# Kernel optimization log

Hardware: AMD Instinct MI355X
Metric: run time of the kernel (lower is better)

Reference implementation:

```python
import jax, jax.numpy as jnp
import numpy as np

B, S, DM = 4, 2048, 1024
H, HD = 16, 64  # num_heads, head_dimension


def setup_inputs() -> dict:
    key = jax.random.key(0)
    ks = jax.random.split(key, 11)
    s = 0.02
    return {
        "queries": jax.random.normal(ks[0], (B, S, DM), dtype=jnp.float32),
        "keys": jax.random.normal(ks[1], (B, S, DM), dtype=jnp.float32),
        "values": jax.random.normal(ks[2], (B, S, DM), dtype=jnp.float32),
        # projection params, stored [in, out] (transpose of torch Linear weight)
        "Wq": jax.random.normal(ks[3], (DM, H * HD), dtype=jnp.float32) * s,
        "bq": jnp.zeros((H * HD,), dtype=jnp.float32),
        "Wk": jax.random.normal(ks[4], (DM, H * HD), dtype=jnp.float32) * s,
        "bk": jnp.zeros((H * HD,), dtype=jnp.float32),
        "Wv": jax.random.normal(ks[5], (DM, H * HD), dtype=jnp.float32) * s,
        "bv": jnp.zeros((H * HD,), dtype=jnp.float32),
        "Wo": jax.random.normal(ks[6], (H * HD, DM), dtype=jnp.float32) * s,
        "bo": jnp.zeros((DM,), dtype=jnp.float32),
    }


def reference(queries, keys, values, Wq, bq, Wk, bk, Wv, bv, Wo, bo):
    b, s, _ = queries.shape
    # project and split heads: [b, s, H*HD] -> [b, H, s, HD]
    def split(x):
        return x.reshape(b, s, H, HD).transpose(0, 2, 1, 3)
    q = split(queries @ Wq + bq)
    k = split(keys @ Wk + bk)
    v = split(values @ Wv + bv)
    # raw scores [b, H, sq, sk]
    attn = jnp.einsum("bhqd,bhkd->bhqk", q, k)
    # FAITHFUL to source: mask is a no-op (masked_fill result discarded);
    # softmax over axis=2 (the QUERY axis), then scaled by 1/sqrt(HD) after.
    attn = jax.nn.softmax(attn, axis=2) / jnp.sqrt(jnp.float32(HD))
    out = jnp.einsum("bhqk,bhkd->bhqd", attn, v)  # [b, H, s, HD]
    out = out.transpose(0, 2, 1, 3).reshape(b, s, H * HD)
    return out @ Wo + bo
```

## Files before the change

### kernel.cpp

```cpp
#include <hip/hip_runtime.h>
#include <cstddef>


typedef unsigned short u16t;
typedef __attribute__((ext_vector_type(8))) short short8;
typedef __attribute__((ext_vector_type(4))) float floatx4;
typedef __attribute__((ext_vector_type(4))) unsigned int uintx4;

#define MFMA16(a, b, c) __builtin_amdgcn_mfma_f32_16x16x32_bf16((a), (b), (c), 0, 0, 0)
#define GLDS16(g, l)                                                        \
  __builtin_amdgcn_global_load_lds(                                         \
      (const __attribute__((address_space(1))) unsigned int*)(g),           \
      (__attribute__((address_space(3))) unsigned int*)(l), 16, 0, 0)

#if __has_builtin(__builtin_amdgcn_exp2f)
#define EXP2(x) __builtin_amdgcn_exp2f(x)
#else
#define EXP2(x) __expf(0.69314718f * (x))
#endif

static __device__ __forceinline__ u16t f2bf(float f) {
  union { float f; unsigned u; } v; v.f = f;
  unsigned r = v.u + 0x7FFFu + ((v.u >> 16) & 1u);
  return (u16t)(r >> 16);
}
static __device__ __forceinline__ unsigned pack2(float hi, float lo) {
  union { float f; unsigned u; } a, b; a.f = hi; b.f = lo;
  return __builtin_amdgcn_perm(a.u + 0x8000u, b.u + 0x8000u, 0x07060302u);
}
static __device__ __forceinline__ unsigned cvtpk(float lo, float hi) {
  unsigned r;
  asm("v_cvt_pk_bf16_f32 %0, %1, %2" : "=v"(r) : "v"(lo), "v"(hi));
  return r;
}

static __device__ __forceinline__ int swz(int row, int col) {
  return (((col >> 3) ^ (row & 7)) << 3) | (col & 7);
}

#define SEQ    2048
#define NHEAD  16
#define HDIM   64
#define DMODEL 1024

__global__ __launch_bounds__(256)
void wt_kernel(const float* __restrict__ W0, const float* __restrict__ W1,
               const float* __restrict__ W2, const float* __restrict__ W3,
               u16t* __restrict__ T0, u16t* __restrict__ T1,
               u16t* __restrict__ T2, u16t* __restrict__ T3) {
  int id = blockIdx.x * 256 + threadIdx.x;
  int wsel = id >> 17;
  int r = id & 131071;
  int n = r & 1023;
  int k0 = (r >> 10) << 3;
  const float* W = wsel == 0 ? W0 : wsel == 1 ? W1 : wsel == 2 ? W2 : W3;
  u16t* T = wsel == 0 ? T0 : wsel == 1 ? T1 : wsel == 2 ? T2 : T3;
  const float* src = W + (size_t)k0 * 1024 + n;
  float f[8];
#pragma unroll
  for (int i = 0; i < 8; ++i) f[i] = src[(size_t)i * 1024];
  uint4 p;
  p.x = pack2(f[1], f[0]); p.y = pack2(f[3], f[2]);
  p.z = pack2(f[5], f[4]); p.w = pack2(f[7], f[6]);
  *(uint4*)&T[(size_t)n * 1024 + (k0 & ~63) + swz(n, k0 & 63)] = p;
}

__global__ __launch_bounds__(256)
void cvt_kernel(const float* __restrict__ X0, const float* __restrict__ X1,
                u16t* __restrict__ T0, u16t* __restrict__ T1) {
  int id = blockIdx.x * 256 + threadIdx.x;
  int wsel = id >> 20;
  int r = id & 1048575;
  int m = r >> 7;
  int k0 = (r & 127) << 3;
  const float* X = wsel == 0 ? X0 : X1;
  u16t* T = wsel == 0 ? T0 : T1;
  const float4* src = (const float4*)(X + (size_t)m * 1024 + k0);
  float4 a = src[0], b = src[1];
  uint4 p;
  p.x = pack2(a.y, a.x); p.y = pack2(a.w, a.z);
  p.z = pack2(b.y, b.x); p.w = pack2(b.w, b.z);
  *(uint4*)&T[(size_t)m * 1024 + (k0 & ~63) + swz(m, k0 & 63)] = p;
}

template <int MODE>
__global__ __launch_bounds__(256)
void gemm_bt(const void* __restrict__ Ap0, const void* __restrict__ Ap1,
             const u16t* __restrict__ BT0, const u16t* __restrict__ BT1,
             const float* __restrict__ bias0, const float* __restrict__ bias1,
             void* __restrict__ Cp0, void* __restrict__ Cp1,
             float sc0, float sc1, const float* __restrict__ sscv) {
  constexpr int K = 1024;
  __shared__ __align__(16) u16t lA[128 * 64];
  __shared__ __align__(16) u16t lB[128 * 64];
  const int z = blockIdx.z;
  const void* Ap = z ? Ap1 : Ap0;
  const u16t* BT = z ? BT1 : BT0;
  const float* bias = z ? bias1 : bias0;
  void* Cp = z ? Cp1 : Cp0;
  const float qsc = z ? sc1 : sc0;
  const int tid = threadIdx.x;
  const int lane = tid & 63, w = tid >> 6;
  const int wm = w >> 1, wn = w & 1;
  const int lrow = lane & 15, lq = lane >> 4;
  const int raw = blockIdx.y * 8 + blockIdx.x;
  const int xcd = raw & 7, slot = raw >> 3;
  const int m0 = (xcd * 8 + (slot >> 3)) * 128;
  const int n0 = (slot & 7) * 128;

  floatx4 acc[4][4];
#pragma unroll
  for (int i = 0; i < 4; ++i)
#pragma unroll
    for (int j = 0; j < 4; ++j) acc[i][j] = {0.f, 0.f, 0.f, 0.f};

  for (int kb = 0; kb < K; kb += 64) {
    if constexpr (MODE == 2) {
      const float* Ag = (const float*)Ap;
#pragma unroll
      for (int i = 0; i < 8; ++i) {
        int e = (i * 256 + tid) * 4;
        int r = e >> 6, c = e & 63;
        const float* src = Ag + (size_t)(m0 + r) * K + kb + c;
        uint2 p;
        p.x = pack2(src[1], src[0]);
        p.y = pack2(src[3], src[2]);
        *(uint2*)&lA[r * 64 + swz(r, c)] = p;
      }
    } else {
      const u16t* Ag = (const u16t*)Ap;
#pragma unroll
      for (int i = 0; i < 4; ++i) {
        int chunk = w * 4 + i;
        int off = chunk * 1024 + lane * 16;
        int r = off >> 7, ib = off & 127;
        GLDS16(Ag + (size_t)(m0 + r) * K + kb + (ib >> 1), &lA[chunk * 512]);
      }
    }
#pragma unroll
    for (int i = 0; i < 4; ++i) {
      int chunk = w * 4 + i;
      int off = chunk * 1024 + lane * 16;
      int r = off >> 7, ib = off & 127;
      GLDS16(BT + (size_t)(n0 + r) * K + kb + (ib >> 1), &lB[chunk * 512]);
    }
    __syncthreads();
#pragma unroll
    for (int kk = 0; kk < 2; ++kk) {
      short8 af[4], bfr[4];
#pragma unroll
      for (int t = 0; t < 4; ++t) {
        int ar = wm * 64 + t * 16 + lrow;
        af[t] = *(const short8*)&lA[ar * 64 + swz(ar, kk * 32 + lq * 8)];
      }
#pragma unroll
      for (int t = 0; t < 4; ++t) {
        int br = wn * 64 + t * 16 + lrow;
        bfr[t] = *(const short8*)&lB[br * 64 + swz(br, kk * 32 + lq * 8)];
      }
#pragma unroll
      for (int i = 0; i < 4; ++i)
#pragma unroll
        for (int j = 0; j < 4; ++j)
          acc[i][j] = MFMA16(af[i], bfr[j], acc[i][j]);
    }
    __syncthreads();
  }

  float bvv[4];
#pragma unroll
  for (int j = 0; j < 4; ++j) bvv[j] = bias[n0 + wn * 64 + j * 16 + lrow];
  const int h = (n0 + wn * 64) >> 6;
#pragma unroll
  for (int i = 0; i < 4; ++i) {
#pragma unroll
    for (int r = 0; r < 4; ++r) {
      int rg = m0 + wm * 64 + i * 16 + lq * 4 + r;
      int b = rg >> 11, s = rg & 2047;
      float rs;
      if constexpr (MODE == 2) rs = sscv[(size_t)(b * NHEAD + h) * SEQ + s];
      else                     rs = qsc;
#pragma unroll
      for (int j = 0; j < 4; ++j) {
        int cg = n0 + wn * 64 + j * 16 + lrow;
        float v = acc[i][j][r] + bvv[j];
        if constexpr (MODE == 1) {
          ((float*)Cp)[(size_t)rg * 1024 + cg] = v;
        } else {
          v *= rs;
          int d = cg & 63;
          size_t bh = (size_t)(b * NHEAD + h);
          if constexpr (MODE == 0) {
            ((u16t*)Cp)[(bh * SEQ + s) * HDIM + swz(s, d)] = f2bf(v);
          } else {
            int sp = (s & ~31) | (((s >> 2) & 3) << 3) | (s & 3) |
                     (((s >> 4) & 1) << 2);
            ((u16t*)Cp)[(bh * HDIM + d) * SEQ + (s & ~127) + swz(d, sp & 127)] =
                f2bf(v);
          }
        }
      }
    }
  }
}

__global__ __launch_bounds__(256)
void stats_kernel(const u16t* __restrict__ Qb, const u16t* __restrict__ Kb,
                  float* __restrict__ ss) {
  __shared__ __align__(16) u16t lK[128 * 64];
  __shared__ __align__(16) u16t lQ[128 * 64];
  const int tid = threadIdx.x, lane = tid & 63, w = tid >> 6;
  const int lrow = lane & 15, lq = lane >> 4;
  const int bh = blockIdx.x;
  const int c0 = blockIdx.y * 128;
  const u16t* Kbase = Kb + (size_t)bh * (SEQ * HDIM);
  const u16t* Qbase = Qb + (size_t)bh * (SEQ * HDIM);

#pragma unroll
  for (int i = 0; i < 4; ++i) {
    int chunk = w * 4 + i;
    GLDS16(Kbase + (size_t)c0 * HDIM + chunk * 512 + lane * 8, &lK[chunk * 512]);
  }

  short8 bfK[4];
  float lcur[2] = {0.f, 0.f};

  for (int q0 = 0; q0 < SEQ; q0 += 128) {
#pragma unroll
    for (int i = 0; i < 4; ++i) {
      int chunk = w * 4 + i;
      GLDS16(Qbase + (size_t)q0 * HDIM + chunk * 512 + lane * 8, &lQ[chunk * 512]);
    }
    __syncthreads();
    if (q0 == 0) {
#pragma unroll
      for (int nt = 0; nt < 2; ++nt) {
        int kr = w * 32 + nt * 16 + lrow;
        bfK[nt * 2]     = *(const short8*)&lK[kr * 64 + swz(kr, lq * 8)];
        bfK[nt * 2 + 1] = *(const short8*)&lK[kr * 64 + swz(kr, lq * 8 + 32)];
      }
    }
#pragma unroll
    for (int mt = 0; mt < 8; ++mt) {
      int qr = mt * 16 + lrow;
      short8 af0 = *(const short8*)&lQ[qr * 64 + swz(qr, lq * 8)];
      short8 af1 = *(const short8*)&lQ[qr * 64 + swz(qr, lq * 8 + 32)];
#pragma unroll
      for (int nt = 0; nt < 2; ++nt) {
        floatx4 a = {0.f, 0.f, 0.f, 0.f};
        a = MFMA16(af0, bfK[nt * 2], a);
        a = MFMA16(af1, bfK[nt * 2 + 1], a);
        lcur[nt] += EXP2(a[0]) + EXP2(a[1]) + EXP2(a[2]) + EXP2(a[3]);
      }
    }
    __syncthreads();
  }
#pragma unroll
  for (int t = 0; t < 2; ++t) {
    float ll = lcur[t];
    ll += __shfl_xor(ll, 16);
    ll += __shfl_xor(ll, 32);
    lcur[t] = ll;
  }
  if (lane < 16) {
#pragma unroll
    for (int t = 0; t < 2; ++t) {
      int col = c0 + w * 32 + t * 16 + lane;
      ss[(size_t)bh * SEQ + col] = 1.f / (8.f * lcur[t]);
    }
  }
}

__global__ __launch_bounds__(256, 2)
void attn_kernel(const u16t* __restrict__ Qb, const u16t* __restrict__ Kb,
                 const u16t* __restrict__ Vt, u16t* __restrict__ Hout) {
  __shared__ __align__(16) u16t sK[2][8192];
  __shared__ __align__(16) u16t sV[2][8192];
  const int tid = threadIdx.x, lane = tid & 63, w = tid >> 6;
  const int lrow = lane & 15, lq = lane >> 4;
  const int bh = blockIdx.x, q0 = blockIdx.y * 256;
  const size_t hb = (size_t)bh * (SEQ * HDIM);

  auto stage = [&](int t) {
    u16t* dK = sK[t & 1];
    u16t* dV = sV[t & 1];
    const int k0 = t << 7;
#pragma unroll
    for (int i = 0; i < 4; ++i) {
      int chunk = w * 4 + i;
      GLDS16(Kb + hb + (size_t)k0 * HDIM + chunk * 512 + lane * 8, &dK[chunk * 512]);
    }
#pragma unroll
    for (int i = 0; i < 4; ++i) {
      int chunk = w * 4 + i;
      int off = chunk * 1024 + lane * 16;
      int d = off >> 8, ib = off & 255;
      GLDS16(Vt + hb + ((size_t)d << 11) + k0 + (ib >> 1), &dV[chunk * 512]);
    }
  };
  auto loadK = [&](short8 dst[2][2], const u16t* K_, int kw) {
#pragma unroll
    for (int t = 0; t < 2; ++t) {
      int kr = (kw * 2 + t) * 16 + lrow;
      dst[t][0] = *(const short8*)&K_[kr * 64 + swz(kr, lq * 8)];
      dst[t][1] = *(const short8*)&K_[kr * 64 + swz(kr, lq * 8 + 32)];
    }
  };
  auto loadV = [&](short8 dst[4], const u16t* V_, int kw) {
#pragma unroll
    for (int dt = 0; dt < 4; ++dt) {
      int vr = dt * 16 + lrow;
      dst[dt] = *(const short8*)&V_[vr * 128 + swz(vr, kw * 32 + lq * 8)];
    }
  };

  u16t* qs = (u16t*)sK;
#pragma unroll
  for (int i = 0; i < 8; ++i) {
    int chunk = w * 8 + i;
    GLDS16(Qb + hb + (size_t)q0 * HDIM + chunk * 512 + lane * 8, &qs[chunk * 512]);
  }
  __syncthreads();
  short8 bq[4][2];
#pragma unroll
  for (int j = 0; j < 4; ++j) {
    int qr = w * 64 + j * 16 + lrow;
    bq[j][0] = *(const short8*)&qs[qr * 64 + swz(qr, lq * 8)];
    bq[j][1] = *(const short8*)&qs[qr * 64 + swz(qr, lq * 8 + 32)];
  }
  __syncthreads();

  floatx4 ao[4][4];
#pragma unroll
  for (int j = 0; j < 4; ++j)
#pragma unroll
    for (int t = 0; t < 4; ++t) ao[j][t] = {0.f, 0.f, 0.f, 0.f};

  stage(0);
  stage(1);

#pragma unroll 2
  for (int kt = 0; kt < 16; ++kt) {
    if (kt < 15) asm volatile("s_waitcnt vmcnt(8)" ::: "memory");
    else         asm volatile("s_waitcnt vmcnt(0)" ::: "memory");
    __builtin_amdgcn_s_barrier();
    const u16t* K_ = sK[kt & 1];
    const u16t* V_ = sV[kt & 1];

    short8 ak[2][2][2];
    short8 bv[2][4];
    loadK(ak[0], K_, 0);
    loadV(bv[0], V_, 0);

#pragma unroll
    for (int kw = 0; kw < 4; ++kw) {
      const int cb = kw & 1, nb = cb ^ 1;
      if (kw < 3) {
        loadK(ak[nb], K_, kw + 1);
        loadV(bv[nb], V_, kw + 1);
      }
      short8 pa[4];
#pragma unroll
      for (int j = 0; j < 4; ++j) {
        floatx4 s0 = {0.f, 0.f, 0.f, 0.f}, s1 = {0.f, 0.f, 0.f, 0.f};
        __builtin_amdgcn_s_setprio(1);
        s0 = MFMA16(ak[cb][0][0], bq[j][0], s0);
        s0 = MFMA16(ak[cb][0][1], bq[j][1], s0);
        s1 = MFMA16(ak[cb][1][0], bq[j][0], s1);
        s1 = MFMA16(ak[cb][1][1], bq[j][1], s1);
        __builtin_amdgcn_s_setprio(0);
        uintx4 pw;
        pw[0] = cvtpk(EXP2(s0[0]), EXP2(s0[1]));
        pw[1] = cvtpk(EXP2(s0[2]), EXP2(s0[3]));
        pw[2] = cvtpk(EXP2(s1[0]), EXP2(s1[1]));
        pw[3] = cvtpk(EXP2(s1[2]), EXP2(s1[3]));
        pa[j] = __builtin_bit_cast(short8, pw);
      }
      __builtin_amdgcn_s_setprio(1);
#pragma unroll
      for (int dt = 0; dt < 4; ++dt)
#pragma unroll
        for (int j = 0; j < 4; ++j)
          ao[j][dt] = MFMA16(pa[j], bv[cb][dt], ao[j][dt]);
      __builtin_amdgcn_s_setprio(0);
    }

    asm volatile("s_waitcnt lgkmcnt(0)" ::: "memory");
    __builtin_amdgcn_s_barrier();
    if (kt < 14) stage(kt + 2);
  }

  const int b = bh >> 4, h = bh & 15;
#pragma unroll
  for (int j = 0; j < 4; ++j)
#pragma unroll
    for (int dt = 0; dt < 4; ++dt) {
      int d = dt * 16 + lrow;
#pragma unroll
      for (int r = 0; r < 4; ++r) {
        int q = q0 + w * 64 + j * 16 + lq * 4 + r;
        Hout[((size_t)b * SEQ + q) * DMODEL + h * HDIM + swz(q, d)] = f2bf(ao[j][dt][r]);
      }
    }
}

extern "C" void kernel_launch(void* const* d_in, const int* in_sizes, int n_in,
                              void* d_out, int out_size, void* d_ws, size_t ws_size,
                              hipStream_t stream) {
  (void)in_sizes; (void)n_in; (void)out_size; (void)ws_size;
  const float* queries = (const float*)d_in[0];
  const float* keys    = (const float*)d_in[1];
  const float* values  = (const float*)d_in[2];
  const float* Wq = (const float*)d_in[3];
  const float* bq = (const float*)d_in[4];
  const float* Wk = (const float*)d_in[5];
  const float* bk = (const float*)d_in[6];
  const float* Wv = (const float*)d_in[7];
  const float* bv = (const float*)d_in[8];
  const float* Wo = (const float*)d_in[9];
  const float* bo = (const float*)d_in[10];

  char* ws = (char*)d_ws;
  const size_t MB = 1024 * 1024;
  u16t* Qb   = (u16t*)(ws + 0 * MB);
  u16t* Kb   = (u16t*)(ws + 16 * MB);
  u16t* qcv  = (u16t*)(ws + 32 * MB);
  u16t* Hout = qcv;
  u16t* kcv  = (u16t*)(ws + 48 * MB);
  u16t* Vt   = kcv;
  u16t* wqt  = (u16t*)(ws + 64 * MB);
  u16t* wkt  = (u16t*)(ws + 66 * MB);
  u16t* wvt  = (u16t*)(ws + 68 * MB);
  u16t* wot  = (u16t*)(ws + 70 * MB);
  float* ssc = (float*)(ws + 72 * MB);

  wt_kernel<<<2048, 256, 0, stream>>>(Wq, Wk, Wv, Wo, wqt, wkt, wvt, wot);

  cvt_kernel<<<8192, 256, 0, stream>>>(queries, keys, qcv, kcv);

  gemm_bt<0><<<dim3(8, 64, 2), 256, 0, stream>>>(
      qcv, kcv, wqt, wkt, bq, bk, Qb, Kb, 1.44269504f, 1.0f, nullptr);

  stats_kernel<<<dim3(64, 16), 256, 0, stream>>>(Qb, Kb, ssc);

  gemm_bt<2><<<dim3(8, 64, 1), 256, 0, stream>>>(
      values, values, wvt, wvt, bv, bv, Vt, Vt, 1.0f, 1.0f, ssc);

  attn_kernel<<<dim3(64, 8), 256, 0, stream>>>(Qb, Kb, Vt, Hout);

  gemm_bt<1><<<dim3(8, 64, 1), 256, 0, stream>>>(
      Hout, Hout, wot, wot, bo, bo, d_out, d_out, 1.0f, 1.0f, nullptr);
}
```

Before: 379.8 us.

## Software-pipeline QK and exp across kw steps; pre-convert values to bf16

Inside the attention loop, the QK^T MFMAs for the next key sub-tile are now issued before the PV MFMAs of the current one. The exp/convert epilogue runs afterwards, so transcendental work can overlap matrix-core work. Separately, the V projection GEMM no longer converts fp32 values to bf16 inline with scalar loads. A dedicated cvt_kernel pass now pre-converts them, which lets that GEMM use the same direct global-to-LDS loads as the other modes. This adds an extra kernel launch and a round trip through memory, and the extra live score registers may raise register pressure.

Measured after the change: 377.4 us. About the same (-0.6%).

```diff
diff --git a/kernel.cpp b/kernel.cpp
--- a/kernel.cpp
+++ b/kernel.cpp
@@ -66,15 +66,10 @@
 }
 
 __global__ __launch_bounds__(256)
-void cvt_kernel(const float* __restrict__ X0, const float* __restrict__ X1,
-                u16t* __restrict__ T0, u16t* __restrict__ T1) {
+void cvt_kernel(const float* __restrict__ X, u16t* __restrict__ T) {
   int id = blockIdx.x * 256 + threadIdx.x;
-  int wsel = id >> 20;
-  int r = id & 1048575;
-  int m = r >> 7;
-  int k0 = (r & 127) << 3;
-  const float* X = wsel == 0 ? X0 : X1;
-  u16t* T = wsel == 0 ? T0 : T1;
+  int m = id >> 7;
+  int k0 = (id & 127) << 3;
   const float4* src = (const float4*)(X + (size_t)m * 1024 + k0);
   float4 a = src[0], b = src[1];
   uint4 p;
@@ -85,7 +80,7 @@
 
 template <int MODE>
 __global__ __launch_bounds__(256)
-void gemm_bt(const void* __restrict__ Ap0, const void* __restrict__ Ap1,
+void gemm_bt(const u16t* __restrict__ Ap0, const u16t* __restrict__ Ap1,
              const u16t* __restrict__ BT0, const u16t* __restrict__ BT1,
              const float* __restrict__ bias0, const float* __restrict__ bias1,
              void* __restrict__ Cp0, void* __restrict__ Cp1,
@@ -94,7 +89,7 @@
   __shared__ __align__(16) u16t lA[128 * 64];
   __shared__ __align__(16) u16t lB[128 * 64];
   const int z = blockIdx.z;
-  const void* Ap = z ? Ap1 : Ap0;
+  const u16t* Ag = z ? Ap1 : Ap0;
   const u16t* BT = z ? BT1 : BT0;
   const float* bias = z ? bias1 : bias0;
   void* Cp = z ? Cp1 : Cp0;
@@ -115,33 +110,12 @@
     for (int j = 0; j < 4; ++j) acc[i][j] = {0.f, 0.f, 0.f, 0.f};
 
   for (int kb = 0; kb < K; kb += 64) {
-    if constexpr (MODE == 2) {
-      const float* Ag = (const float*)Ap;
-#pragma unroll
-      for (int i = 0; i < 8; ++i) {
-        int e = (i * 256 + tid) * 4;
-        int r = e >> 6, c = e & 63;
-        const float* src = Ag + (size_t)(m0 + r) * K + kb + c;
-        uint2 p;
-        p.x = pack2(src[1], src[0]);
-        p.y = pack2(src[3], src[2]);
-        *(uint2*)&lA[r * 64 + swz(r, c)] = p;
-      }
-    } else {
-      const u16t* Ag = (const u16t*)Ap;
-#pragma unroll
-      for (int i = 0; i < 4; ++i) {
-        int chunk = w * 4 + i;
-        int off = chunk * 1024 + lane * 16;
-        int r = off >> 7, ib = off & 127;
-        GLDS16(Ag + (size_t)(m0 + r) * K + kb + (ib >> 1), &lA[chunk * 512]);
-      }
-    }
 #pragma unroll
     for (int i = 0; i < 4; ++i) {
       int chunk = w * 4 + i;
       int off = chunk * 1024 + lane * 16;
       int r = off >> 7, ib = off & 127;
+      GLDS16(Ag + (size_t)(m0 + r) * K + kb + (ib >> 1), &lA[chunk * 512]);
       GLDS16(BT + (size_t)(n0 + r) * K + kb + (ib >> 1), &lB[chunk * 512]);
     }
     __syncthreads();
@@ -330,6 +304,31 @@
   }
   __syncthreads();
 
+  auto qk = [&](const short8 ak[2][2], floatx4 s[4][2]) {
+    __builtin_amdgcn_s_setprio(1);
+#pragma unroll
+    for (int j = 0; j < 4; ++j) {
+      floatx4 a = {0.f, 0.f, 0.f, 0.f}, b = {0.f, 0.f, 0.f, 0.f};
+      a = MFMA16(ak[0][0], bq[j][0], a);
+      a = MFMA16(ak[0][1], bq[j][1], a);
+      b = MFMA16(ak[1][0], bq[j][0], b);
+      b = MFMA16(ak[1][1], bq[j][1], b);
+      s[j][0] = a; s[j][1] = b;
+    }
+    __builtin_amdgcn_s_setprio(0);
+  };
+  auto ep = [&](const floatx4 s[4][2], short8 pa[4]) {
+#pragma unroll
+    for (int j = 0; j < 4; ++j) {
+      uintx4 pw;
+      pw[0] = cvtpk(EXP2(s[j][0][0]), EXP2(s[j][0][1]));
+      pw[1] = cvtpk(EXP2(s[j][0][2]), EXP2(s[j][0][3]));
+      pw[2] = cvtpk(EXP2(s[j][1][0]), EXP2(s[j][1][1]));
+      pw[3] = cvtpk(EXP2(s[j][1][2]), EXP2(s[j][1][3]));
+      pa[j] = __builtin_bit_cast(short8, pw);
+    }
+  };
+
   floatx4 ao[4][4];
 #pragma unroll
   for (int j = 0; j < 4; ++j)
@@ -347,42 +346,36 @@
     const u16t* K_ = sK[kt & 1];
     const u16t* V_ = sV[kt & 1];
 
-    short8 ak[2][2][2];
-    short8 bv[2][4];
-    loadK(ak[0], K_, 0);
-    loadV(bv[0], V_, 0);
+    short8 ak0[2][2];
+    loadK(ak0, K_, 0);
+    floatx4 s0[4][2];
+    qk(ak0, s0);
+    short8 pa[4];
+    ep(s0, pa);
 
 #pragma unroll
     for (int kw = 0; kw < 4; ++kw) {
-      const int cb = kw & 1, nb = cb ^ 1;
+      short8 bv[4];
+      loadV(bv, V_, kw);
+      short8 akN[2][2];
+      floatx4 sN[4][2];
       if (kw < 3) {
-        loadK(ak[nb], K_, kw + 1);
-        loadV(bv[nb], V_, kw + 1);
-      }
-      short8 pa[4];
-#pragma unroll
-      for (int j = 0; j < 4; ++j) {
-        floatx4 s0 = {0.f, 0.f, 0.f, 0.f}, s1 = {0.f, 0.f, 0.f, 0.f};
-        __builtin_amdgcn_s_setprio(1);
-        s0 = MFMA16(ak[cb][0][0], bq[j][0], s0);
-        s0 = MFMA16(ak[cb][0][1], bq[j][1], s0);
-        s1 = MFMA16(ak[cb][1][0], bq[j][0], s1);
-        s1 = MFMA16(ak[cb][1][1], bq[j][1], s1);
-        __builtin_amdgcn_s_setprio(0);
-        uintx4 pw;
-        pw[0] = cvtpk(EXP2(s0[0]), EXP2(s0[1]));
-        pw[1] = cvtpk(EXP2(s0[2]), EXP2(s0[3]));
-        pw[2] = cvtpk(EXP2(s1[0]), EXP2(s1[1]));
-        pw[3] = cvtpk(EXP2(s1[2]), EXP2(s1[3]));
-        pa[j] = __builtin_bit_cast(short8, pw);
+        loadK(akN, K_, kw + 1);
+        qk(akN, sN);
       }
       __builtin_amdgcn_s_setprio(1);
 #pragma unroll
       for (int dt = 0; dt < 4; ++dt)
 #pragma unroll
         for (int j = 0; j < 4; ++j)
-          ao[j][dt] = MFMA16(pa[j], bv[cb][dt], ao[j][dt]);
+          ao[j][dt] = MFMA16(pa[j], bv[dt], ao[j][dt]);
       __builtin_amdgcn_s_setprio(0);
+      if (kw < 3) {
+        short8 paN[4];
+        ep(sN, paN);
+#pragma unroll
+        for (int j = 0; j < 4; ++j) pa[j] = paN[j];
+      }
     }
 
     asm volatile("s_waitcnt lgkmcnt(0)" ::: "memory");
@@ -425,6 +418,7 @@
   u16t* Qb   = (u16t*)(ws + 0 * MB);
   u16t* Kb   = (u16t*)(ws + 16 * MB);
   u16t* qcv  = (u16t*)(ws + 32 * MB);
+  u16t* vcv  = qcv;
   u16t* Hout = qcv;
   u16t* kcv  = (u16t*)(ws + 48 * MB);
   u16t* Vt   = kcv;
@@ -436,15 +430,18 @@
 
   wt_kernel<<<2048, 256, 0, stream>>>(Wq, Wk, Wv, Wo, wqt, wkt, wvt, wot);
 
-  cvt_kernel<<<8192, 256, 0, stream>>>(queries, keys, qcv, kcv);
+  cvt_kernel<<<4096, 256, 0, stream>>>(queries, qcv);
+  cvt_kernel<<<4096, 256, 0, stream>>>(keys, kcv);
 
   gemm_bt<0><<<dim3(8, 64, 2), 256, 0, stream>>>(
       qcv, kcv, wqt, wkt, bq, bk, Qb, Kb, 1.44269504f, 1.0f, nullptr);
 
+  cvt_kernel<<<4096, 256, 0, stream>>>(values, vcv);
+
   stats_kernel<<<dim3(64, 16), 256, 0, stream>>>(Qb, Kb, ssc);
 
   gemm_bt<2><<<dim3(8, 64, 1), 256, 0, stream>>>(
-      values, values, wvt, wvt, bv, bv, Vt, Vt, 1.0f, 1.0f, ssc);
+      vcv, vcv, wvt, wvt, bv, bv, Vt, Vt, 1.0f, 1.0f, ssc);
 
   attn_kernel<<<dim3(64, 8), 256, 0, stream>>>(Qb, Kb, Vt, Hout);
 
```
